# Kernel tuning notes

Hardware: AMD Instinct MI355X
Metric: run time of the kernel (lower is better)

## Reference

```python
import jax, jax.numpy as jnp
from jax import lax
import numpy as np

K_SIZE = 3  # SteerableKernelBase.create_radial(3)


def _radial_basis_3x3():
    """Orthonormal radial steerable basis on a 3x3 grid.
    Returns 6 unit-norm kernels: [k0_center, k0_ring, k1_cos, k1_sin, k2_cos, k2_sin]."""
    ys, xs = np.mgrid[-1:2, -1:2].astype(np.float32)
    ang = np.arctan2(ys, xs)
    ring = (np.hypot(xs, ys) > 0).astype(np.float32)

    def unit(k):
        return (k / np.linalg.norm(k)).astype(np.float32)

    b0c = np.zeros((3, 3), np.float32); b0c[1, 1] = 1.0
    basis = np.stack([
        b0c,                       # k=0, r=0
        unit(ring),                # k=0, r=1
        unit(np.cos(ang) * ring),  # k=1 real
        unit(np.sin(ang) * ring),  # k=1 imag
        unit(np.cos(2 * ang) * ring),  # k=2 real
        unit(np.sin(2 * ang) * ring),  # k=2 imag
    ])
    return jnp.asarray(basis)  # (6, 3, 3)


def setup_inputs() -> dict:
    key = jax.random.key(0)
    k1, k2, k3 = jax.random.split(key, 3)
    N, C_in, C_out, H, W = 16, 64, 64, 128, 128
    x = jax.random.normal(k1, (N, C_in, H, W), dtype=jnp.float32)
    # steering angle field in [0,1); alpha = (cos 2*pi*theta, sin 2*pi*theta) is unitary
    theta = jax.random.uniform(k2, (N, 1, H, W), dtype=jnp.float32)
    # steerable weights: (n_out, n_in, 4) -> [k0 center, k0 ring, k1, k2]
    fan_in = C_in * K_SIZE * K_SIZE
    std = jnp.sqrt(2.0 / fan_in)  # relu gain init as in steerable_base.init_weights
    weights = jax.random.normal(k3, (C_out, C_in, 4), dtype=jnp.float32) * std
    bias = jnp.zeros((C_out,), dtype=jnp.float32)
    return {"x": x, "theta": theta, "weights": weights, "bias": bias}


def reference(x, theta, weights, bias):
    basis = _radial_basis_3x3()  # (6,3,3)
    O = weights.shape[0]
    w = weights[..., None, None]  # (O,I,4,1,1)
    # Synthesize per-harmonic kernels (O,I,3,3) from the steerable basis
    k0 = w[:, :, 0] * basis[0] + w[:, :, 1] * basis[1]
    k1r = w[:, :, 2] * basis[2]
    k1i = w[:, :, 2] * basis[3]
    k2r = w[:, :, 3] * basis[4]
    k2i = w[:, :, 3] * basis[5]
    ker = jnp.concatenate([k0, k1r, k1i, k2r, k2i], axis=0)  # (5O, I, 3, 3)

    z = lax.conv_general_dilated(
        x, ker, window_strides=(1, 1), padding="SAME",
        dimension_numbers=("NCHW", "OIHW", "NCHW"))  # (N, 5O, H, W)
    N, _, H, W = z.shape
    z = z.reshape(N, 5, O, H, W)

    # angle harmonics cos(k*alpha), sin(k*alpha); alpha unitary so rho=1 path
    a = 2.0 * jnp.pi * theta  # (N,1,H,W)
    c1, s1 = jnp.cos(a), jnp.sin(a)
    c2 = 2.0 * c1 * c1 - 1.0
    s2 = 2.0 * s1 * c1

    out = (z[:, 0] + c1 * z[:, 1] + s1 * z[:, 2]
           + c2 * z[:, 3] + s2 * z[:, 4])
    return out + bias[None, :, None, None]
```

## Files before the change

kernel.cpp:

```cpp
#include <hip/hip_runtime.h>


typedef __bf16 bf16x8 __attribute__((ext_vector_type(8)));
typedef float  f32x16 __attribute__((ext_vector_type(16)));
typedef unsigned int u32;
typedef const __attribute__((address_space(1))) u32* gp_t;
typedef __attribute__((address_space(3))) u32* lp_t;

#define HH 128
#define WW 128
#define TILE_H 8
#define TILE_W 32
#define CHCH 8
#define NCHUNK 8
#define RROWS 10
#define RCOLS 40
#define CHF (RROWS * RCOLS)
#define CHIMG 65536

__global__ void wt_to_bf16(const float* __restrict__ wt,
                           unsigned short* __restrict__ wb) {
    int i = blockIdx.x * 256 + threadIdx.x;
    union { float f; u32 u; } v; v.f = wt[i];
    wb[i] = (unsigned short)((v.u + 0x7FFF + ((v.u >> 16) & 1)) >> 16);
}

__global__ __launch_bounds__(256, 4) void steered_conv_mfma(
    const float* __restrict__ x, const float* __restrict__ theta,
    const unsigned short* __restrict__ wb, const float* __restrict__ bias,
    float* __restrict__ out)
{
    __shared__ float lds[2][CHCH][CHF];

    const int tid  = threadIdx.x;
    const int wid  = tid >> 6, lane = tid & 63;
    const int pc   = lane & 31, hx = lane >> 5;

    const int bb  = blockIdx.x;
    const int swz = (bb & 7) * 128 + (bb >> 3);
    const int n  = swz >> 6;
    const int ty = (swz >> 2) & 15;
    const int tx = swz & 3;
    const int h0 = ty * TILE_H, w0 = tx * TILE_W;
    const int p0 = wid * 2;

    const int oA = lane * 16;
    const int rA = oA / 160;
    const int cA = oA - rA * 160;
    int ghA = h0 - 1 + rA; ghA = ghA < 0 ? 0 : (ghA > 127 ? 127 : ghA);
    int srcA = ghA * 512 + w0 * 4 - 16 + cA;
    srcA = srcA < 0 ? 0 : srcA;
    const bool skA = (w0 == 0 && cA < 16) || (w0 == 96 && cA >= 144);

    const int oB = 1024 + lane * 16;
    const int rB = oB / 160;
    const int cB = oB - rB * 160;
    int ghB = h0 - 1 + rB; ghB = ghB < 0 ? 0 : (ghB > 127 ? 127 : ghB);
    int srcB = ghB * 512 + w0 * 4 - 16 + cB;
    srcB = srcB < 0 ? 0 : (srcB > CHIMG - 16 ? CHIMG - 16 : srcB);
    const bool skB = (lane >= 36) || (w0 == 0 && cB < 16) || (w0 == 96 && cB >= 144);

    const char* xn = (const char*)x + (size_t)n * 64 * CHIMG;
    const bool boundary = (h0 == 0) | (h0 == 120) | (w0 == 0) | (w0 == 96);

    #pragma unroll
    for (int j = 0; j < 2; ++j) {
        const int ch = wid * 2 + j;
        const char* s = xn + ch * CHIMG;
        char* d = (char*)&lds[0][ch][0];
        if (!skA) __builtin_amdgcn_global_load_lds((gp_t)(s + srcA), (lp_t)d, 16, 0, 0);
        if (!skB) __builtin_amdgcn_global_load_lds((gp_t)(s + srcB), (lp_t)(d + 1024), 16, 0, 0);
    }

    const int wg = w0 + pc;
    const float thA = theta[(n * HH + h0 + p0) * WW + wg];
    const float thB = theta[(n * HH + h0 + p0 + 1) * WW + wg];
    float s1a, c1a, s1b, c1b;
    __sincosf(6.2831853071795864769f * thA, &s1a, &c1a);
    __sincosf(6.2831853071795864769f * thB, &s1b, &c1b);
    const float c2a = 2.f * c1a * c1a - 1.f, s2a = 2.f * s1a * c1a;
    const float c2b = 2.f * c1b * c1b - 1.f, s2b = 2.f * s1b * c1b;

    f32x16 acc00, acc01, acc10, acc11;
    #pragma unroll
    for (int r = 0; r < 16; ++r) { acc00[r]=0.f; acc01[r]=0.f; acc10[r]=0.f; acc11[r]=0.f; }

    const float RS  = 0.35355339059327373f;
    const float HMR = 0.14644660940672627f;

    #pragma unroll 1
    for (int c = 0; c < NCHUNK; ++c) {
        __syncthreads();
        if (boundary) {
            float* bz = &lds[c & 1][0][0];
            if (h0 == 0)
                for (int i = tid; i < CHCH * RCOLS; i += 256) bz[(i / RCOLS) * CHF + (i % RCOLS)] = 0.f;
            if (h0 == 120)
                for (int i = tid; i < CHCH * RCOLS; i += 256) bz[(i / RCOLS) * CHF + 9 * RCOLS + (i % RCOLS)] = 0.f;
            if (w0 == 0)
                for (int i = tid; i < CHCH * RROWS; i += 256) bz[(i / RROWS) * CHF + (i % RROWS) * RCOLS + 3] = 0.f;
            if (w0 == 96)
                for (int i = tid; i < CHCH * RROWS; i += 256) bz[(i / RROWS) * CHF + (i % RROWS) * RCOLS + 36] = 0.f;
            __syncthreads();
        }
        if (c < NCHUNK - 1) {
            const char* xc = xn + (size_t)(c + 1) * CHCH * CHIMG;
            #pragma unroll
            for (int j = 0; j < 2; ++j) {
                const int ch = wid * 2 + j;
                const char* s = xc + ch * CHIMG;
                char* d = (char*)&lds[(c + 1) & 1][ch][0];
                if (!skA) __builtin_amdgcn_global_load_lds((gp_t)(s + srcA), (lp_t)d, 16, 0, 0);
                if (!skB) __builtin_amdgcn_global_load_lds((gp_t)(s + srcB), (lp_t)(d + 1024), 16, 0, 0);
            }
        }
        const float* tb = &lds[c & 1][0][p0 * RCOLS + pc + 3];
        const unsigned short* wk = wb + pc * 256 + c * 32 + hx * 8;
        #pragma unroll
        for (int kc = 0; kc < 2; ++kc) {
            bf16x8 b0, b1;
            #pragma unroll
            for (int cs = 0; cs < 2; ++cs) {
                const float* t = tb + (kc * 4 + hx * 2 + cs) * CHF;
                const float t00=t[0],   t01=t[1],   t02=t[2];
                const float t10=t[40],  t11=t[41],  t12=t[42];
                const float t20=t[80],  t21=t[81],  t22=t[82];
                const float t30=t[120], t31=t[121], t32=t[122];
                const float S0=t00+t01+t02, S1=t10+t11+t12;
                const float S2=t20+t21+t22, S3=t30+t31+t32;
                const float D0=t02-t00, D1=t12-t10, D2=t22-t20, D3=t32-t30;
                {
                    const float F1 = RS * (S0 + S2 + S1 - t11);
                    const float B2 = RS * (D0 + D2) + 0.5f * D1;
                    const float B3 = RS * (S2 - S0) + HMR * (t21 - t01);
                    const float B4 = 0.5f * (S1 - t11 - t01 - t21);
                    const float B5 = 0.5f * (D2 - D0);
                    b0[cs*4+0] = (__bf16)t11;
                    b0[cs*4+1] = (__bf16)F1;
                    b0[cs*4+2] = (__bf16)(c1a * B2 + s1a * B3);
                    b0[cs*4+3] = (__bf16)(c2a * B4 + s2a * B5);
                }
                {
                    const float F1 = RS * (S1 + S3 + S2 - t21);
                    const float B2 = RS * (D1 + D3) + 0.5f * D2;
                    const float B3 = RS * (S3 - S1) + HMR * (t31 - t11);
                    const float B4 = 0.5f * (S2 - t21 - t11 - t31);
                    const float B5 = 0.5f * (D3 - D1);
                    b1[cs*4+0] = (__bf16)t21;
                    b1[cs*4+1] = (__bf16)F1;
                    b1[cs*4+2] = (__bf16)(c1b * B2 + s1b * B3);
                    b1[cs*4+3] = (__bf16)(c2b * B4 + s2b * B5);
                }
            }
            const unsigned short* wr = wk + kc * 16;
            const bf16x8 A0 = *(const bf16x8*)wr;
            const bf16x8 A1 = *(const bf16x8*)(wr + 32 * 256);
            acc00 = __builtin_amdgcn_mfma_f32_32x32x16_bf16(A0, b0, acc00, 0, 0, 0);
            acc01 = __builtin_amdgcn_mfma_f32_32x32x16_bf16(A1, b0, acc01, 0, 0, 0);
            acc10 = __builtin_amdgcn_mfma_f32_32x32x16_bf16(A0, b1, acc10, 0, 0, 0);
            acc11 = __builtin_amdgcn_mfma_f32_32x32x16_bf16(A1, b1, acc11, 0, 0, 0);
        }
    }

    const size_t hw = (size_t)HH * WW;
    float* op = out + (size_t)n * 64 * hw + (size_t)(h0 + p0) * WW + w0 + pc;
    #pragma unroll
    for (int r = 0; r < 16; ++r) {
        const int o  = (r & 3) + 8 * (r >> 2) + 4 * hx;
        const float bo = bias[o], bo2 = bias[o + 32];
        op[(size_t)o * hw]             = acc00[r] + bo;
        op[(size_t)(o + 32) * hw]      = acc01[r] + bo2;
        op[(size_t)o * hw + WW]        = acc10[r] + bo;
        op[(size_t)(o + 32) * hw + WW] = acc11[r] + bo2;
    }
}

extern "C" void kernel_launch(void* const* d_in, const int* in_sizes, int n_in,
                              void* d_out, int out_size, void* d_ws, size_t ws_size,
                              hipStream_t stream) {
    const float* x     = (const float*)d_in[0];
    const float* theta = (const float*)d_in[1];
    const float* wt    = (const float*)d_in[2];
    const float* bias  = (const float*)d_in[3];
    float* out = (float*)d_out;
    unsigned short* wb = (unsigned short*)d_ws;

    wt_to_bf16<<<64, 256, 0, stream>>>(wt, wb);

    steered_conv_mfma<<<1024, 256, 0, stream>>>(x, theta, wb, bias, out);
}
```

Baseline: 42.92 us.

## Triple-buffer input staging with vmcnt waits and repacked weight layout

```diff
diff --git a/kernel.cpp b/kernel.cpp
--- a/kernel.cpp
+++ b/kernel.cpp
@@ -3,26 +3,29 @@
 
 typedef __bf16 bf16x8 __attribute__((ext_vector_type(8)));
 typedef float  f32x16 __attribute__((ext_vector_type(16)));
+typedef float  f32x4  __attribute__((ext_vector_type(4)));
 typedef unsigned int u32;
 typedef const __attribute__((address_space(1))) u32* gp_t;
 typedef __attribute__((address_space(3))) u32* lp_t;
 
 #define HH 128
 #define WW 128
-#define TILE_H 8
-#define TILE_W 32
 #define CHCH 8
 #define NCHUNK 8
+#define NBUF 3
 #define RROWS 10
 #define RCOLS 40
-#define CHF (RROWS * RCOLS)
+#define CHF 400
 #define CHIMG 65536
 
-__global__ void wt_to_bf16(const float* __restrict__ wt,
-                           unsigned short* __restrict__ wb) {
+__global__ void wt_repack(const float* __restrict__ wt,
+                          unsigned short* __restrict__ wb) {
     int i = blockIdx.x * 256 + threadIdx.x;
+    int o = i >> 8, k = i & 255;
     union { float f; u32 u; } v; v.f = wt[i];
-    wb[i] = (unsigned short)((v.u + 0x7FFF + ((v.u >> 16) & 1)) >> 16);
+    unsigned short b = (unsigned short)((v.u + 0x7FFF + ((v.u >> 16) & 1)) >> 16);
+    int kcg = k >> 4, hxx = (k >> 3) & 1, r = k & 7;
+    wb[((kcg * 2 + hxx) * 64 + o) * 8 + r] = b;
 }
 
 __global__ __launch_bounds__(256, 4) void steered_conv_mfma(
@@ -30,18 +33,17 @@
     const unsigned short* __restrict__ wb, const float* __restrict__ bias,
     float* __restrict__ out)
 {
-    __shared__ float lds[2][CHCH][CHF];
+    __shared__ __attribute__((aligned(16))) float lds[NBUF][CHCH][CHF];
 
-    const int tid  = threadIdx.x;
-    const int wid  = tid >> 6, lane = tid & 63;
-    const int pc   = lane & 31, hx = lane >> 5;
+    const int tid = threadIdx.x;
+    const int wid = tid >> 6, lane = tid & 63;
+    const int pc = lane & 31, hx = lane >> 5;
 
-    const int bb  = blockIdx.x;
+    const int bb = blockIdx.x;
     const int swz = (bb & 7) * 128 + (bb >> 3);
-    const int n  = swz >> 6;
-    const int ty = (swz >> 2) & 15;
-    const int tx = swz & 3;
-    const int h0 = ty * TILE_H, w0 = tx * TILE_W;
+    const int n = swz >> 6;
+    const int ty = (swz >> 2) & 15, tx = swz & 3;
+    const int h0 = ty * 8, w0 = tx * 32;
     const int p0 = wid * 2;
 
     const int oA = lane * 16;
@@ -50,7 +52,8 @@
     int ghA = h0 - 1 + rA; ghA = ghA < 0 ? 0 : (ghA > 127 ? 127 : ghA);
     int srcA = ghA * 512 + w0 * 4 - 16 + cA;
     srcA = srcA < 0 ? 0 : srcA;
-    const bool skA = (w0 == 0 && cA < 16) || (w0 == 96 && cA >= 144);
+    const bool skA = (w0 == 0 && cA < 16) || (w0 == 96 && cA >= 144)
+                   || (h0 == 0 && rA == 0);
 
     const int oB = 1024 + lane * 16;
     const int rB = oB / 160;
@@ -58,28 +61,38 @@
     int ghB = h0 - 1 + rB; ghB = ghB < 0 ? 0 : (ghB > 127 ? 127 : ghB);
     int srcB = ghB * 512 + w0 * 4 - 16 + cB;
     srcB = srcB < 0 ? 0 : (srcB > CHIMG - 16 ? CHIMG - 16 : srcB);
-    const bool skB = (lane >= 36) || (w0 == 0 && cB < 16) || (w0 == 96 && cB >= 144);
+    const bool skB = (lane >= 36) || (w0 == 0 && cB < 16) || (w0 == 96 && cB >= 144)
+                   || (h0 == 120 && rB == 9);
 
     const char* xn = (const char*)x + (size_t)n * 64 * CHIMG;
-    const bool boundary = (h0 == 0) | (h0 == 120) | (w0 == 0) | (w0 == 96);
 
-    #pragma unroll
-    for (int j = 0; j < 2; ++j) {
-        const int ch = wid * 2 + j;
-        const char* s = xn + ch * CHIMG;
-        char* d = (char*)&lds[0][ch][0];
-        if (!skA) __builtin_amdgcn_global_load_lds((gp_t)(s + srcA), (lp_t)d, 16, 0, 0);
-        if (!skB) __builtin_amdgcn_global_load_lds((gp_t)(s + srcB), (lp_t)(d + 1024), 16, 0, 0);
+    float s1a, c1a, s1b, c1b;
+    __sincosf(6.2831853071795864769f * theta[(n*HH + h0+p0)*WW + w0+pc], &s1a, &c1a);
+    __sincosf(6.2831853071795864769f * theta[(n*HH + h0+p0+1)*WW + w0+pc], &s1b, &c1b);
+    const float c2a = 2.f*c1a*c1a - 1.f, s2a = 2.f*s1a*c1a;
+    const float c2b = 2.f*c1b*c1b - 1.f, s2b = 2.f*s1b*c1b;
+
+    if ((h0 == 0) | (h0 == 120) | (w0 == 0) | (w0 == 96)) {
+        f32x4* z = (f32x4*)&lds[0][0][0];
+        for (int i = tid; i < NBUF * CHCH * CHF / 4; i += 256)
+            z[i] = f32x4{0.f, 0.f, 0.f, 0.f};
     }
+    __syncthreads();
 
-    const int wg = w0 + pc;
-    const float thA = theta[(n * HH + h0 + p0) * WW + wg];
-    const float thB = theta[(n * HH + h0 + p0 + 1) * WW + wg];
-    float s1a, c1a, s1b, c1b;
-    __sincosf(6.2831853071795864769f * thA, &s1a, &c1a);
-    __sincosf(6.2831853071795864769f * thB, &s1b, &c1b);
-    const float c2a = 2.f * c1a * c1a - 1.f, s2a = 2.f * s1a * c1a;
-    const float c2b = 2.f * c1b * c1b - 1.f, s2b = 2.f * s1b * c1b;
+    auto stage = [&](int t) {
+        const char* xc = xn + (size_t)(t * CHCH) * CHIMG;
+        #pragma unroll
+        for (int j = 0; j < 2; ++j) {
+            const int ch = wid * 2 + j;
+            const char* s = xc + ch * CHIMG;
+            char* d = (char*)&lds[t % NBUF][ch][0];
+            if (!skA) __builtin_amdgcn_global_load_lds((gp_t)(s + srcA), (lp_t)d, 16, 0, 0);
+            if (!skB) __builtin_amdgcn_global_load_lds((gp_t)(s + srcB), (lp_t)(d + 1024), 16, 0, 0);
+        }
+    };
+
+    stage(0);
+    stage(1);
 
     f32x16 acc00, acc01, acc10, acc11;
     #pragma unroll
@@ -87,35 +100,22 @@
 
     const float RS  = 0.35355339059327373f;
     const float HMR = 0.14644660940672627f;
+    const unsigned short* wbl = wb + (hx * 64 + pc) * 8;
 
-    #pragma unroll 1
+    #pragma unroll
     for (int c = 0; c < NCHUNK; ++c) {
-        __syncthreads();
-        if (boundary) {
-            float* bz = &lds[c & 1][0][0];
-            if (h0 == 0)
-                for (int i = tid; i < CHCH * RCOLS; i += 256) bz[(i / RCOLS) * CHF + (i % RCOLS)] = 0.f;
-            if (h0 == 120)
-                for (int i = tid; i < CHCH * RCOLS; i += 256) bz[(i / RCOLS) * CHF + 9 * RCOLS + (i % RCOLS)] = 0.f;
-            if (w0 == 0)
-                for (int i = tid; i < CHCH * RROWS; i += 256) bz[(i / RROWS) * CHF + (i % RROWS) * RCOLS + 3] = 0.f;
-            if (w0 == 96)
-                for (int i = tid; i < CHCH * RROWS; i += 256) bz[(i / RROWS) * CHF + (i % RROWS) * RCOLS + 36] = 0.f;
-            __syncthreads();
-        }
-        if (c < NCHUNK - 1) {
-            const char* xc = xn + (size_t)(c + 1) * CHCH * CHIMG;
-            #pragma unroll
-            for (int j = 0; j < 2; ++j) {
-                const int ch = wid * 2 + j;
-                const char* s = xc + ch * CHIMG;
-                char* d = (char*)&lds[(c + 1) & 1][ch][0];
-                if (!skA) __builtin_amdgcn_global_load_lds((gp_t)(s + srcA), (lp_t)d, 16, 0, 0);
-                if (!skB) __builtin_amdgcn_global_load_lds((gp_t)(s + srcB), (lp_t)(d + 1024), 16, 0, 0);
-            }
-        }
-        const float* tb = &lds[c & 1][0][p0 * RCOLS + pc + 3];
-        const unsigned short* wk = wb + pc * 256 + c * 32 + hx * 8;
+        asm volatile("s_waitcnt vmcnt(4)" ::: "memory");
+        const unsigned short* wr0 = wbl + c * 2048;
+        const bf16x8 A00 = *(const bf16x8*)(wr0);
+        const bf16x8 A01 = *(const bf16x8*)(wr0 + 256);
+        const bf16x8 A10 = *(const bf16x8*)(wr0 + 1024);
+        const bf16x8 A11 = *(const bf16x8*)(wr0 + 1280);
+        __builtin_amdgcn_sched_barrier(0);
+        __builtin_amdgcn_s_barrier();
+        if (c < NCHUNK - 2) stage(c + 2);
+        __builtin_amdgcn_sched_barrier(0);
+
+        const float* tb = &lds[c % NBUF][0][p0 * RCOLS + pc + 3];
         #pragma unroll
         for (int kc = 0; kc < 2; ++kc) {
             bf16x8 b0, b1;
@@ -152,13 +152,14 @@
                     b1[cs*4+3] = (__bf16)(c2b * B4 + s2b * B5);
                 }
             }
-            const unsigned short* wr = wk + kc * 16;
-            const bf16x8 A0 = *(const bf16x8*)wr;
-            const bf16x8 A1 = *(const bf16x8*)(wr + 32 * 256);
+            const bf16x8 A0 = kc ? A10 : A00;
+            const bf16x8 A1 = kc ? A11 : A01;
+            __builtin_amdgcn_s_setprio(1);
             acc00 = __builtin_amdgcn_mfma_f32_32x32x16_bf16(A0, b0, acc00, 0, 0, 0);
             acc01 = __builtin_amdgcn_mfma_f32_32x32x16_bf16(A1, b0, acc01, 0, 0, 0);
             acc10 = __builtin_amdgcn_mfma_f32_32x32x16_bf16(A0, b1, acc10, 0, 0, 0);
             acc11 = __builtin_amdgcn_mfma_f32_32x32x16_bf16(A1, b1, acc11, 0, 0, 0);
+            __builtin_amdgcn_s_setprio(0);
         }
     }
 
@@ -166,7 +167,7 @@
     float* op = out + (size_t)n * 64 * hw + (size_t)(h0 + p0) * WW + w0 + pc;
     #pragma unroll
     for (int r = 0; r < 16; ++r) {
-        const int o  = (r & 3) + 8 * (r >> 2) + 4 * hx;
+        const int o = (r & 3) + 8 * (r >> 2) + 4 * hx;
         const float bo = bias[o], bo2 = bias[o + 32];
         op[(size_t)o * hw]             = acc00[r] + bo;
         op[(size_t)(o + 32) * hw]      = acc01[r] + bo2;
@@ -185,7 +186,7 @@
     float* out = (float*)d_out;
     unsigned short* wb = (unsigned short*)d_ws;
 
-    wt_to_bf16<<<64, 256, 0, stream>>>(wt, wb);
+    wt_repack<<<64, 256, 0, stream>>>(wt, wb);
 
     steered_conv_mfma<<<1024, 256, 0, stream>>>(x, theta, wb, bias, out);
 }
```

New measurement: 41.91 us. -2.3%, faster.
